# Performance work log

Hardware: AMD Instinct MI355X
Metric: run time of the kernel (lower is better)

The kernel has to match this reference:

```python
import jax, jax.numpy as jnp
import numpy as np

H, W = 128, 128          # input_shape
OUT_H, OUT_W = 64, 64    # output_shape -> n_samples = 4096


def setup_inputs() -> dict:
    key = jax.random.key(0)
    k1, k2, k3 = jax.random.split(key, 3)
    activations = jax.random.normal(k1, (8, H, W), dtype=jnp.float32)
    mu = jax.random.uniform(k2, (OUT_H * OUT_W, 2), dtype=jnp.float32)
    sigma = jax.random.uniform(k3, (OUT_H * OUT_W, 2), dtype=jnp.float32)
    return {"activations": activations, "mu": mu, "sigma": sigma}


def reference(activations, mu, sigma):
    # coordinate grid: arange(dim)/dim per axis, range [0, 1)
    gh = jnp.arange(H, dtype=jnp.float32) / H          # [H]
    gw = jnp.arange(W, dtype=jnp.float32) / W          # [W]
    inv2s2 = 1.0 / (2.0 * jnp.square(sigma))           # [N, 2]
    # separable exponent: sum over dims splits into h-part + w-part
    eh = jnp.square(gh[:, None] - mu[None, :, 0]) * inv2s2[None, :, 0]  # [H, N]
    ew = jnp.square(gw[:, None] - mu[None, :, 1]) * inv2s2[None, :, 1]  # [W, N]
    pdf = jnp.exp(-(eh[:, None, :] + ew[None, :, :]))  # [H, W, N]
    # mean over spatial dims of pdf * activations (fused contraction)
    corr = jnp.einsum('bhw,hwn->bn', activations, pdf) / (H * W)  # [B, N]
    return corr.reshape(activations.shape[0], OUT_H, OUT_W)
```

## Files before the change

### kernel.cpp

```cpp
#include <hip/hip_runtime.h>

#define NOUT 4096

typedef _Float16 f16x8 __attribute__((ext_vector_type(8)));
typedef __fp16   h16x2 __attribute__((ext_vector_type(2)));
typedef __fp16   h16x4 __attribute__((ext_vector_type(4)));
typedef __fp16   h16x8 __attribute__((ext_vector_type(8)));
typedef float    f32x4 __attribute__((ext_vector_type(4)));

__device__ __forceinline__ f16x8 cat4(h16x2 a, h16x2 b, h16x2 c, h16x2 d) {
    h16x4 ab = __builtin_shufflevector(a, b, 0, 1, 2, 3);
    h16x4 cd = __builtin_shufflevector(c, d, 0, 1, 2, 3);
    h16x8 v  = __builtin_shufflevector(ab, cd, 0, 1, 2, 3, 4, 5, 6, 7);
    return __builtin_bit_cast(f16x8, v);
}

__device__ __forceinline__ void cvtfrag(float4 p0, float4 p1, f16x8& hi, f16x8& lo) {
    h16x2 h0 = __builtin_amdgcn_cvt_pkrtz(p0.x, p0.y);
    h16x2 h1 = __builtin_amdgcn_cvt_pkrtz(p0.z, p0.w);
    h16x2 h2 = __builtin_amdgcn_cvt_pkrtz(p1.x, p1.y);
    h16x2 h3 = __builtin_amdgcn_cvt_pkrtz(p1.z, p1.w);
    h16x2 l0 = __builtin_amdgcn_cvt_pkrtz(p0.x - (float)h0[0], p0.y - (float)h0[1]);
    h16x2 l1 = __builtin_amdgcn_cvt_pkrtz(p0.z - (float)h1[0], p0.w - (float)h1[1]);
    h16x2 l2 = __builtin_amdgcn_cvt_pkrtz(p1.x - (float)h2[0], p1.y - (float)h2[1]);
    h16x2 l3 = __builtin_amdgcn_cvt_pkrtz(p1.z - (float)h3[0], p1.w - (float)h3[1]);
    hi = cat4(h0, h1, h2, h3);
    lo = cat4(l0, l1, l2, l3);
}

__global__ __launch_bounds__(256, 4) void gauss_fused_kernel(
    const float* __restrict__ act,
    const float* __restrict__ mu,
    const float* __restrict__ sigma,
    float* __restrict__ out)
{
    __shared__ f16x8  EwLDS[16][64];
    __shared__ float4 musig[32];
    __shared__ float  red[4][32];

    const int t    = threadIdx.x;
    const int wv   = t >> 6;
    const int lane = t & 63;
    const int lm   = lane & 15;
    const int lg   = lane >> 4;
    const int n0   = blockIdx.x * 32;
    const int b    = blockIdx.y;
    const float* Ab = act + b * 16384;

    const int h0 = wv * 32 + lm, h1 = h0 + 16;
    const float* r0 = Ab + h0 * 128 + lg * 8;
    const float* r1 = Ab + h1 * 128 + lg * 8;
    float4 pf[2][2][2];
    #pragma unroll
    for (int s = 0; s < 2; ++s) {
        pf[s][0][0] = *reinterpret_cast<const float4*>(r0 + s * 32);
        pf[s][0][1] = *reinterpret_cast<const float4*>(r0 + s * 32 + 4);
        pf[s][1][0] = *reinterpret_cast<const float4*>(r1 + s * 32);
        pf[s][1][1] = *reinterpret_cast<const float4*>(r1 + s * 32 + 4);
    }

    if (t < 32) {
        float2 m = reinterpret_cast<const float2*>(mu)[n0 + t];
        float2 s = reinterpret_cast<const float2*>(sigma)[n0 + t];
        musig[t] = make_float4(m.x, m.y, 0.5f / (s.x * s.x), 0.5f / (s.y * s.y));
    }

    const int ksg = t >> 6;
    #pragma unroll
    for (int mf = 0; mf < 2; ++mf) {
        int n = n0 + mf * 16 + lm;
        float2 m = reinterpret_cast<const float2*>(mu)[n];
        float2 s = reinterpret_cast<const float2*>(sigma)[n];
        float c = 0.5f / (s.y * s.y);
        int w0 = ksg * 32 + lg * 8;
        float e[8];
        #pragma unroll
        for (int j = 0; j < 8; ++j) {
            float d = (float)(w0 + j) * (1.0f / 128.0f) - m.y;
            e[j] = __expf(-d * d * c);
        }
        f16x8 hi, lo;
        cvtfrag(make_float4(e[0], e[1], e[2], e[3]),
                make_float4(e[4], e[5], e[6], e[7]), hi, lo);
        EwLDS[(ksg * 2 + mf) * 2 + 0][lane] = hi;
        EwLDS[(ksg * 2 + mf) * 2 + 1][lane] = lo;
    }
    __syncthreads();

    f32x4 acc[2][2] = {};
    #pragma unroll
    for (int ks = 0; ks < 4; ++ks) {
        const int cur = ks & 1;
        f16x8 ah0, al0, ah1, al1;
        cvtfrag(pf[cur][0][0], pf[cur][0][1], ah0, al0);
        cvtfrag(pf[cur][1][0], pf[cur][1][1], ah1, al1);
        if (ks < 2) {
            pf[cur][0][0] = *reinterpret_cast<const float4*>(r0 + (ks + 2) * 32);
            pf[cur][0][1] = *reinterpret_cast<const float4*>(r0 + (ks + 2) * 32 + 4);
            pf[cur][1][0] = *reinterpret_cast<const float4*>(r1 + (ks + 2) * 32);
            pf[cur][1][1] = *reinterpret_cast<const float4*>(r1 + (ks + 2) * 32 + 4);
        }
        #pragma unroll
        for (int mf = 0; mf < 2; ++mf) {
            f16x8 ewh = EwLDS[(ks * 2 + mf) * 2 + 0][lane];
            f16x8 ewl = EwLDS[(ks * 2 + mf) * 2 + 1][lane];
            acc[mf][0] = __builtin_amdgcn_mfma_f32_16x16x32_f16(ewh, ah0, acc[mf][0], 0, 0, 0);
            acc[mf][0] = __builtin_amdgcn_mfma_f32_16x16x32_f16(ewh, al0, acc[mf][0], 0, 0, 0);
            acc[mf][0] = __builtin_amdgcn_mfma_f32_16x16x32_f16(ewl, ah0, acc[mf][0], 0, 0, 0);
            acc[mf][1] = __builtin_amdgcn_mfma_f32_16x16x32_f16(ewh, ah1, acc[mf][1], 0, 0, 0);
            acc[mf][1] = __builtin_amdgcn_mfma_f32_16x16x32_f16(ewh, al1, acc[mf][1], 0, 0, 0);
            acc[mf][1] = __builtin_amdgcn_mfma_f32_16x16x32_f16(ewl, ah1, acc[mf][1], 0, 0, 0);
        }
    }

    const float gh0 = (float)h0 * (1.0f / 128.0f);
    const float gh1 = (float)h1 * (1.0f / 128.0f);
    float s8[2][4];
    #pragma unroll
    for (int mf = 0; mf < 2; ++mf)
        #pragma unroll
        for (int r = 0; r < 4; ++r) {
            int n = mf * 16 + 4 * lg + r;
            float4 ms = musig[n];
            float d0 = gh0 - ms.x, d1 = gh1 - ms.x;
            float e0 = __expf(-d0 * d0 * ms.z);
            float e1 = __expf(-d1 * d1 * ms.z);
            float v = e0 * acc[mf][0][r] + e1 * acc[mf][1][r];
            v += __shfl_xor(v, 1, 64);
            v += __shfl_xor(v, 2, 64);
            v += __shfl_xor(v, 4, 64);
            v += __shfl_xor(v, 8, 64);
            s8[mf][r] = v;
        }
    if (lm == 0) {
        #pragma unroll
        for (int mf = 0; mf < 2; ++mf)
            #pragma unroll
            for (int r = 0; r < 4; ++r)
                red[wv][mf * 16 + 4 * lg + r] = s8[mf][r];
    }
    __syncthreads();

    if (t < 32) {
        float s = red[0][t] + red[1][t] + red[2][t] + red[3][t];
        out[b * NOUT + n0 + t] = s * (1.0f / 16384.0f);
    }
}

extern "C" void kernel_launch(void* const* d_in, const int* in_sizes, int n_in,
                              void* d_out, int out_size, void* d_ws, size_t ws_size,
                              hipStream_t stream) {
    const float* act   = (const float*)d_in[0];
    const float* mu    = (const float*)d_in[1];
    const float* sigma = (const float*)d_in[2];
    float* out = (float*)d_out;

    dim3 grid(NOUT / 32, 8);
    gauss_fused_kernel<<<grid, 256, 0, stream>>>(act, mu, sigma, out);
}
```

Baseline: 14.66 us.

## Widen output tile to 64 samples with 512-thread blocks, one h-row per wave

Each block now covers 64 output samples with 8 waves, each wave owning 16 rows of H instead of 32. Every activation fragment is reused across four sample fragments instead of two. This halves the number of times the activation image is re-read and converted to split fp16 across blocks. In exchange the grid has half as many blocks (512), each with more LDS and a larger final reduction over 8 waves.

Result: faster. 13.23 us (median of 2 runs) (-9.8%).

```diff
diff --git a/kernel.cpp b/kernel.cpp
--- a/kernel.cpp
+++ b/kernel.cpp
@@ -28,121 +28,117 @@
     lo = cat4(l0, l1, l2, l3);
 }
 
-__global__ __launch_bounds__(256, 4) void gauss_fused_kernel(
+__global__ __launch_bounds__(512, 4) void gauss_fused64_kernel(
     const float* __restrict__ act,
     const float* __restrict__ mu,
     const float* __restrict__ sigma,
     float* __restrict__ out)
 {
-    __shared__ f16x8  EwLDS[16][64];
-    __shared__ float4 musig[32];
-    __shared__ float  red[4][32];
+    __shared__ f16x8  EwLDS[16][2][64];
+    __shared__ float4 musig[64];
+    __shared__ float  red[8][64];
 
     const int t    = threadIdx.x;
     const int wv   = t >> 6;
     const int lane = t & 63;
     const int lm   = lane & 15;
     const int lg   = lane >> 4;
-    const int n0   = blockIdx.x * 32;
+    const int n0   = blockIdx.x * 64;
     const int b    = blockIdx.y;
     const float* Ab = act + b * 16384;
 
-    const int h0 = wv * 32 + lm, h1 = h0 + 16;
-    const float* r0 = Ab + h0 * 128 + lg * 8;
-    const float* r1 = Ab + h1 * 128 + lg * 8;
-    float4 pf[2][2][2];
-    #pragma unroll
-    for (int s = 0; s < 2; ++s) {
-        pf[s][0][0] = *reinterpret_cast<const float4*>(r0 + s * 32);
-        pf[s][0][1] = *reinterpret_cast<const float4*>(r0 + s * 32 + 4);
-        pf[s][1][0] = *reinterpret_cast<const float4*>(r1 + s * 32);
-        pf[s][1][1] = *reinterpret_cast<const float4*>(r1 + s * 32 + 4);
-    }
-
-    if (t < 32) {
+    const int cA = 2 * wv, cB = 2 * wv + 1;
+    float2 mA = reinterpret_cast<const float2*>(mu)[n0 + (cA & 3) * 16 + lm];
+    float2 sA = reinterpret_cast<const float2*>(sigma)[n0 + (cA & 3) * 16 + lm];
+    float2 mB = reinterpret_cast<const float2*>(mu)[n0 + (cB & 3) * 16 + lm];
+    float2 sB = reinterpret_cast<const float2*>(sigma)[n0 + (cB & 3) * 16 + lm];
+    if (t < 64) {
         float2 m = reinterpret_cast<const float2*>(mu)[n0 + t];
         float2 s = reinterpret_cast<const float2*>(sigma)[n0 + t];
         musig[t] = make_float4(m.x, m.y, 0.5f / (s.x * s.x), 0.5f / (s.y * s.y));
     }
 
-    const int ksg = t >> 6;
+    const int h = wv * 16 + lm;
+    const float* r0 = Ab + h * 128 + lg * 8;
+    float4 pf[2][2];
     #pragma unroll
-    for (int mf = 0; mf < 2; ++mf) {
-        int n = n0 + mf * 16 + lm;
-        float2 m = reinterpret_cast<const float2*>(mu)[n];
-        float2 s = reinterpret_cast<const float2*>(sigma)[n];
-        float c = 0.5f / (s.y * s.y);
-        int w0 = ksg * 32 + lg * 8;
+    for (int s = 0; s < 2; ++s) {
+        pf[s][0] = *reinterpret_cast<const float4*>(r0 + s * 32);
+        pf[s][1] = *reinterpret_cast<const float4*>(r0 + s * 32 + 4);
+    }
+
+    #pragma unroll
+    for (int i = 0; i < 2; ++i) {
+        const int c  = 2 * wv + i;
+        const int ks = c >> 2;
+        const int w0 = ks * 32 + lg * 8;
+        float2 m = i ? mB : mA;
+        float2 s = i ? sB : sA;
+        float cc = 0.5f / (s.y * s.y);
         float e[8];
         #pragma unroll
         for (int j = 0; j < 8; ++j) {
             float d = (float)(w0 + j) * (1.0f / 128.0f) - m.y;
-            e[j] = __expf(-d * d * c);
+            e[j] = __expf(-d * d * cc);
         }
         f16x8 hi, lo;
         cvtfrag(make_float4(e[0], e[1], e[2], e[3]),
                 make_float4(e[4], e[5], e[6], e[7]), hi, lo);
-        EwLDS[(ksg * 2 + mf) * 2 + 0][lane] = hi;
-        EwLDS[(ksg * 2 + mf) * 2 + 1][lane] = lo;
+        EwLDS[c][0][lane] = hi;
+        EwLDS[c][1][lane] = lo;
     }
     __syncthreads();
 
-    f32x4 acc[2][2] = {};
+    f32x4 acc[4] = {};
     #pragma unroll
     for (int ks = 0; ks < 4; ++ks) {
         const int cur = ks & 1;
-        f16x8 ah0, al0, ah1, al1;
-        cvtfrag(pf[cur][0][0], pf[cur][0][1], ah0, al0);
-        cvtfrag(pf[cur][1][0], pf[cur][1][1], ah1, al1);
+        f16x8 ah, al;
+        cvtfrag(pf[cur][0], pf[cur][1], ah, al);
         if (ks < 2) {
-            pf[cur][0][0] = *reinterpret_cast<const float4*>(r0 + (ks + 2) * 32);
-            pf[cur][0][1] = *reinterpret_cast<const float4*>(r0 + (ks + 2) * 32 + 4);
-            pf[cur][1][0] = *reinterpret_cast<const float4*>(r1 + (ks + 2) * 32);
-            pf[cur][1][1] = *reinterpret_cast<const float4*>(r1 + (ks + 2) * 32 + 4);
+            pf[cur][0] = *reinterpret_cast<const float4*>(r0 + (ks + 2) * 32);
+            pf[cur][1] = *reinterpret_cast<const float4*>(r0 + (ks + 2) * 32 + 4);
         }
         #pragma unroll
-        for (int mf = 0; mf < 2; ++mf) {
-            f16x8 ewh = EwLDS[(ks * 2 + mf) * 2 + 0][lane];
-            f16x8 ewl = EwLDS[(ks * 2 + mf) * 2 + 1][lane];
-            acc[mf][0] = __builtin_amdgcn_mfma_f32_16x16x32_f16(ewh, ah0, acc[mf][0], 0, 0, 0);
-            acc[mf][0] = __builtin_amdgcn_mfma_f32_16x16x32_f16(ewh, al0, acc[mf][0], 0, 0, 0);
-            acc[mf][0] = __builtin_amdgcn_mfma_f32_16x16x32_f16(ewl, ah0, acc[mf][0], 0, 0, 0);
-            acc[mf][1] = __builtin_amdgcn_mfma_f32_16x16x32_f16(ewh, ah1, acc[mf][1], 0, 0, 0);
-            acc[mf][1] = __builtin_amdgcn_mfma_f32_16x16x32_f16(ewh, al1, acc[mf][1], 0, 0, 0);
-            acc[mf][1] = __builtin_amdgcn_mfma_f32_16x16x32_f16(ewl, ah1, acc[mf][1], 0, 0, 0);
+        for (int mf = 0; mf < 4; ++mf) {
+            f16x8 ewh = EwLDS[ks * 4 + mf][0][lane];
+            f16x8 ewl = EwLDS[ks * 4 + mf][1][lane];
+            acc[mf] = __builtin_amdgcn_mfma_f32_16x16x32_f16(ewh, ah, acc[mf], 0, 0, 0);
+            acc[mf] = __builtin_amdgcn_mfma_f32_16x16x32_f16(ewh, al, acc[mf], 0, 0, 0);
+            acc[mf] = __builtin_amdgcn_mfma_f32_16x16x32_f16(ewl, ah, acc[mf], 0, 0, 0);
         }
     }
 
-    const float gh0 = (float)h0 * (1.0f / 128.0f);
-    const float gh1 = (float)h1 * (1.0f / 128.0f);
-    float s8[2][4];
+    const float gh = (float)h * (1.0f / 128.0f);
+    float sv[4][4];
     #pragma unroll
-    for (int mf = 0; mf < 2; ++mf)
+    for (int mf = 0; mf < 4; ++mf)
         #pragma unroll
         for (int r = 0; r < 4; ++r) {
             int n = mf * 16 + 4 * lg + r;
             float4 ms = musig[n];
-            float d0 = gh0 - ms.x, d1 = gh1 - ms.x;
-            float e0 = __expf(-d0 * d0 * ms.z);
-            float e1 = __expf(-d1 * d1 * ms.z);
-            float v = e0 * acc[mf][0][r] + e1 * acc[mf][1][r];
+            float d = gh - ms.x;
+            float v = __expf(-d * d * ms.z) * acc[mf][r];
             v += __shfl_xor(v, 1, 64);
             v += __shfl_xor(v, 2, 64);
             v += __shfl_xor(v, 4, 64);
             v += __shfl_xor(v, 8, 64);
-            s8[mf][r] = v;
+            sv[mf][r] = v;
         }
     if (lm == 0) {
         #pragma unroll
-        for (int mf = 0; mf < 2; ++mf)
+        for (int mf = 0; mf < 4; ++mf)
             #pragma unroll
             for (int r = 0; r < 4; ++r)
-                red[wv][mf * 16 + 4 * lg + r] = s8[mf][r];
+                red[wv][mf * 16 + 4 * lg + r] = sv[mf][r];
     }
     __syncthreads();
 
-    if (t < 32) {
-        float s = red[0][t] + red[1][t] + red[2][t] + red[3][t];
+    if (t < 64) {
+        float s = 0.f;
+        #pragma unroll
+        for (int w = 0; w < 8; ++w)
+            s += red[w][t];
         out[b * NOUT + n0 + t] = s * (1.0f / 16384.0f);
     }
 }
@@ -155,6 +151,6 @@
     const float* sigma = (const float*)d_in[2];
     float* out = (float*)d_out;
 
-    dim3 grid(NOUT / 32, 8);
-    gauss_fused_kernel<<<grid, 256, 0, stream>>>(act, mu, sigma, out);
+    dim3 grid(NOUT / 64, 8);
+    gauss_fused64_kernel<<<grid, 512, 0, stream>>>(act, mu, sigma, out);
 }
```
